# Optimization experiments

Measured on AMD Instinct MI355X. Metric: run time of the kernel, lower is better.

The kernel has to match this reference:

```python
import jax, jax.numpy as jnp
import numpy as np

EMBED_DIM = 1024
NUM_HEADS = 16
HEAD_DIM = EMBED_DIM // NUM_HEADS
WINDOW = 128


def setup_inputs() -> dict:
    key = jax.random.key(0)
    ks = jax.random.split(key, 9)
    B, T, C = 1, 2048, EMBED_DIM
    s = 1.0 / np.sqrt(C)
    inp = {
        "x": jax.random.normal(ks[0], (B, T, C), dtype=jnp.float32),
        "wq": jax.random.normal(ks[1], (C, C), dtype=jnp.float32) * s,
        "bq": jnp.zeros((C,), dtype=jnp.float32),
        "wk": jax.random.normal(ks[2], (C, C), dtype=jnp.float32) * s,
        "bk": jnp.zeros((C,), dtype=jnp.float32),
        "wv": jax.random.normal(ks[3], (C, C), dtype=jnp.float32) * s,
        "bv": jnp.zeros((C,), dtype=jnp.float32),
        "wo": jax.random.normal(ks[4], (C, C), dtype=jnp.float32) * s,
        "bo": jnp.zeros((C,), dtype=jnp.float32),
    }
    return inp


def reference(x, wq, bq, wk, bk, wv, bv, wo, bo):
    B, T, C = x.shape
    H, D, W = NUM_HEADS, HEAD_DIM, WINDOW

    def proj(w, b):
        # torch Linear: y = x @ w.T + b ; -> (B, H, T, D)
        return (x @ w.T + b).reshape(B, T, H, D).transpose(0, 2, 1, 3)

    q = proj(wq, bq)
    k = proj(wk, bk)
    v = proj(wv, bv)

    # window index map: position t attends to keys [t-W+1, t]; zero-padded before 0
    idx = jnp.arange(T)[:, None] + jnp.arange(W)[None, :] - (W - 1)  # (T, W)
    valid = (idx >= 0)
    idxc = jnp.clip(idx, 0, T - 1)

    kw = k[:, :, idxc]                                 # (B, H, T, W, D)
    vw = v[:, :, idxc] * valid[None, None, :, :, None]  # zero padded values

    # zero-key padding gives raw score exactly 0 (inside the softmax)
    scores = jnp.einsum('bhtd,bhtwd->bhtw', q, kw)
    scores = jnp.where(valid[None, None], scores, 0.0) / np.sqrt(D)
    attn = jax.nn.softmax(scores, axis=-1)             # (B, H, T, W)

    ctx = jnp.einsum('bhtw,bhtwd->bhtd', attn, vw)     # (B, H, T, D)
    out = ctx.transpose(0, 2, 1, 3).reshape(B, T, C)
    return out @ wo.T + bo
```

## Files before the change

kernel.cpp:

```cpp
#include <hip/hip_runtime.h>


#define TSEQ 2048
#define CDIM 1024
#define HNUM 16
#define DHEAD 64
#define WWIN 128

typedef __attribute__((ext_vector_type(8))) short bf16x8;
typedef __attribute__((ext_vector_type(4))) float f32x4;

__device__ __forceinline__ unsigned short f2bf(float f) {
  unsigned u = __float_as_uint(f);
  u = (u + 0x7fffu + ((u >> 16) & 1u)) >> 16;
  return (unsigned short)u;
}
__device__ __forceinline__ float bf2f(unsigned short s) {
  return __uint_as_float(((unsigned)s) << 16);
}

__device__ __forceinline__ void gload16(const void* g, void* l) {
  __builtin_amdgcn_global_load_lds(
      (const __attribute__((address_space(1))) unsigned int*)g,
      (__attribute__((address_space(3))) unsigned int*)l, 16, 0, 0);
}

__global__ void split_bf16(const float* s0, const float* s1, const float* s2,
                           const float* s3,
                           unsigned short* h0, unsigned short* h1,
                           unsigned short* h2, unsigned short* h3,
                           unsigned short* l0, unsigned short* l1,
                           unsigned short* l2, unsigned short* l3, int n4) {
  const int z = blockIdx.z;
  const float* __restrict__ src = z == 0 ? s0 : (z == 1 ? s1 : (z == 2 ? s2 : s3));
  unsigned short* __restrict__ h = z == 0 ? h0 : (z == 1 ? h1 : (z == 2 ? h2 : h3));
  unsigned short* __restrict__ l = z == 0 ? l0 : (z == 1 ? l1 : (z == 2 ? l2 : l3));
  const int i = blockIdx.x * 256 + threadIdx.x;
  if (i >= n4) return;
  const float4 v = ((const float4*)src)[i];
  ushort4 hh, ll;
  hh.x = f2bf(v.x); ll.x = f2bf(v.x - bf2f(hh.x));
  hh.y = f2bf(v.y); ll.y = f2bf(v.y - bf2f(hh.y));
  hh.z = f2bf(v.z); ll.z = f2bf(v.z - bf2f(hh.z));
  hh.w = f2bf(v.w); ll.w = f2bf(v.w - bf2f(hh.w));
  ((ushort4*)h)[i] = hh;
  ((ushort4*)l)[i] = ll;
}

__launch_bounds__(256, 2)
__global__ void gemm_mfma_split(const unsigned short* __restrict__ Ah,
                                const unsigned short* __restrict__ Al,
                                const unsigned short* Bh0, const unsigned short* Bh1,
                                const unsigned short* Bh2,
                                const unsigned short* Bl0, const unsigned short* Bl1,
                                const unsigned short* Bl2,
                                const float* bias0, const float* bias1, const float* bias2,
                                float* C0, float* C1, float* C2,
                                int M, int N, int K) {
  const int z = blockIdx.z;
  const unsigned short* __restrict__ Bh = z == 0 ? Bh0 : (z == 1 ? Bh1 : Bh2);
  const unsigned short* __restrict__ Bl = z == 0 ? Bl0 : (z == 1 ? Bl1 : Bl2);
  const float* __restrict__ bias = z == 0 ? bias0 : (z == 1 ? bias1 : bias2);
  float* __restrict__ C = z == 0 ? C0 : (z == 1 ? C1 : C2);

  __shared__ unsigned short lAh[64 * 32], lAl[64 * 32];
  __shared__ unsigned short lBh[128 * 32], lBl[128 * 32];

  const int tid = threadIdx.x;
  const int w = tid >> 6, lane = tid & 63;
  const int wr = w >> 1, wc = w & 1;
  const int bm = blockIdx.y * 64, bn = blockIdx.x * 128;

  const int sA = tid;
  const int rA = sA >> 2;
  const int cA = ((sA & 3) ^ ((rA >> 1) & 3)) * 8;
  const int oA = (w * 64) * 8;
  int srowB[2], scolB[2], soffB[2];
#pragma unroll
  for (int q = 0; q < 2; ++q) {
    const int s = w * 128 + q * 64 + lane;
    const int r = s >> 2;
    srowB[q] = r;
    scolB[q] = ((s & 3) ^ ((r >> 1) & 3)) * 8;
    soffB[q] = (w * 128 + q * 64) * 8;
  }
  int aoff[2], boff[4];
#pragma unroll
  for (int i = 0; i < 2; ++i) {
    const int ra = wr * 32 + i * 16 + (lane & 15);
    aoff[i] = ra * 32 + (((lane >> 4) ^ ((ra >> 1) & 3)) * 8);
  }
#pragma unroll
  for (int j = 0; j < 4; ++j) {
    const int rb = wc * 64 + j * 16 + (lane & 15);
    boff[j] = rb * 32 + (((lane >> 4) ^ ((rb >> 1) & 3)) * 8);
  }

  f32x4 acc[2][4];
#pragma unroll
  for (int i = 0; i < 2; ++i)
#pragma unroll
    for (int j = 0; j < 4; ++j) acc[i][j] = {0.f, 0.f, 0.f, 0.f};

  const unsigned short* gAh = Ah + (size_t)bm * K;
  const unsigned short* gAl = Al + (size_t)bm * K;
  const unsigned short* gBh = Bh + (size_t)bn * K;
  const unsigned short* gBl = Bl + (size_t)bn * K;

  for (int k0 = 0; k0 < K; k0 += 32) {
    {
      const size_t goA = (size_t)rA * K + k0 + cA;
      gload16(gAh + goA, &lAh[oA]);
      gload16(gAl + goA, &lAl[oA]);
    }
#pragma unroll
    for (int q = 0; q < 2; ++q) {
      const size_t go = (size_t)srowB[q] * K + k0 + scolB[q];
      gload16(gBh + go, &lBh[soffB[q]]);
      gload16(gBl + go, &lBl[soffB[q]]);
    }
    __syncthreads();

    bf16x8 fah[2], fal[2], fbh[4], fbl[4];
#pragma unroll
    for (int i = 0; i < 2; ++i) {
      fah[i] = *(const bf16x8*)&lAh[aoff[i]];
      fal[i] = *(const bf16x8*)&lAl[aoff[i]];
    }
#pragma unroll
    for (int j = 0; j < 4; ++j) {
      fbh[j] = *(const bf16x8*)&lBh[boff[j]];
      fbl[j] = *(const bf16x8*)&lBl[boff[j]];
    }
#pragma unroll
    for (int i = 0; i < 2; ++i)
#pragma unroll
      for (int j = 0; j < 4; ++j) {
        acc[i][j] = __builtin_amdgcn_mfma_f32_16x16x32_bf16(fah[i], fbh[j], acc[i][j], 0, 0, 0);
        acc[i][j] = __builtin_amdgcn_mfma_f32_16x16x32_bf16(fah[i], fbl[j], acc[i][j], 0, 0, 0);
        acc[i][j] = __builtin_amdgcn_mfma_f32_16x16x32_bf16(fal[i], fbh[j], acc[i][j], 0, 0, 0);
      }
    __syncthreads();
  }

  const int colb = bn + wc * 64 + (lane & 15);
  const int rowb = bm + wr * 32 + ((lane >> 4) << 2);
#pragma unroll
  for (int j = 0; j < 4; ++j) {
    const int col = colb + j * 16;
    const float bv = bias[col];
#pragma unroll
    for (int i = 0; i < 2; ++i) {
      const int row = rowb + i * 16;
#pragma unroll
      for (int r = 0; r < 4; ++r)
        C[(size_t)(row + r) * N + col] = acc[i][j][r] + bv;
    }
  }
}

__launch_bounds__(256, 2)
__global__ void gemm_bt(const float* __restrict__ A,
                        const float* __restrict__ Bw0, const float* __restrict__ Bw1,
                        const float* __restrict__ Bw2,
                        const float* __restrict__ bias0, const float* __restrict__ bias1,
                        const float* __restrict__ bias2,
                        float* __restrict__ C0, float* __restrict__ C1, float* __restrict__ C2,
                        int M, int N, int K) {
  const int z = blockIdx.z;
  const float* __restrict__ B = (z == 0) ? Bw0 : ((z == 1) ? Bw1 : Bw2);
  const float* __restrict__ bias = (z == 0) ? bias0 : ((z == 1) ? bias1 : bias2);
  float* __restrict__ C = (z == 0) ? C0 : ((z == 1) ? C1 : C2);

  __shared__ float As[16][132];
  __shared__ float Bs[16][132];

  const int tid = threadIdx.x;
  const int tx = tid & 15;
  const int ty = tid >> 4;
  const int bm = blockIdx.y * 128;
  const int bn = blockIdx.x * 128;
  const int lrow = tid >> 2;
  const int lk = (tid & 3) << 2;

  float acc[8][8] = {};

  for (int k0 = 0; k0 < K; k0 += 16) {
#pragma unroll
    for (int r = 0; r < 2; ++r) {
      const int row = (r << 6) + lrow;
      const float4 a4 = *(const float4*)(A + (size_t)(bm + row) * K + k0 + lk);
      As[lk + 0][row] = a4.x; As[lk + 1][row] = a4.y;
      As[lk + 2][row] = a4.z; As[lk + 3][row] = a4.w;
      const float4 b4 = *(const float4*)(B + (size_t)(bn + row) * K + k0 + lk);
      Bs[lk + 0][row] = b4.x; Bs[lk + 1][row] = b4.y;
      Bs[lk + 2][row] = b4.z; Bs[lk + 3][row] = b4.w;
    }
    __syncthreads();
#pragma unroll
    for (int k = 0; k < 16; ++k) {
      float a[8], b[8];
      *(float4*)(a)     = *(const float4*)(&As[k][ty * 8]);
      *(float4*)(a + 4) = *(const float4*)(&As[k][ty * 8 + 4]);
      *(float4*)(b)     = *(const float4*)(&Bs[k][tx * 8]);
      *(float4*)(b + 4) = *(const float4*)(&Bs[k][tx * 8 + 4]);
#pragma unroll
      for (int i = 0; i < 8; ++i)
#pragma unroll
        for (int j = 0; j < 8; ++j)
          acc[i][j] = fmaf(a[i], b[j], acc[i][j]);
    }
    __syncthreads();
  }

#pragma unroll
  for (int i = 0; i < 8; ++i) {
    const int row = bm + ty * 8 + i;
#pragma unroll
    for (int j4 = 0; j4 < 2; ++j4) {
      const int col = bn + tx * 8 + j4 * 4;
      const float4 bb = *(const float4*)(bias + col);
      float4 o;
      o.x = acc[i][j4 * 4 + 0] + bb.x;
      o.y = acc[i][j4 * 4 + 1] + bb.y;
      o.z = acc[i][j4 * 4 + 2] + bb.z;
      o.w = acc[i][j4 * 4 + 3] + bb.w;
      *(float4*)(C + (size_t)row * N + col) = o;
    }
  }
}

__launch_bounds__(512)
__global__ void swa_attn(const float* __restrict__ Q, const float* __restrict__ K,
                         const float* __restrict__ V, float* __restrict__ Of,
                         unsigned short* __restrict__ Oh, unsigned short* __restrict__ Ol,
                         int pack) {
  __shared__ float kb[160 * 64];
  __shared__ float qs[32 * 64];
  __shared__ float ps[8 * 4 * 132];

  const int h = blockIdx.y;
  const int t0 = blockIdx.x * 32;
  const int tid = threadIdx.x;
  const int hoff = h * DHEAD;

  for (int i = tid; i < 160 * 16; i += 512) {
    const int x = i >> 4;
    const int cp = i & 15;
    const int c = cp ^ (x & 15);
    const int key = t0 - (WWIN - 1) + x;
    float4 kv = make_float4(0.f, 0.f, 0.f, 0.f);
    if (key >= 0 && key < TSEQ)
      kv = *(const float4*)(K + (size_t)key * CDIM + hoff + 4 * c);
    *(float4*)&kb[x * 64 + 4 * cp] = kv;
  }
  for (int i = tid; i < 32 * 16; i += 512) {
    const int xq = i >> 4;
    const int c = i & 15;
    *(float4*)&qs[xq * 64 + 4 * c] =
        *(const float4*)(Q + (size_t)(t0 + xq) * CDIM + hoff + 4 * c);
  }
  for (int i = tid; i < 8 * 4 * 132; i += 512) ps[i] = 0.f;
  __syncthreads();

  const int w = tid >> 6;
  const int lane = tid & 63;
  const int q0 = w * 4;

  float inv[4];

#pragma unroll
  for (int q = 0; q < 4; ++q) {
    const int xl = q0 + q + lane;
    const int xm = xl & 15;
    const float* kp0 = kb + xl * 64;
    const float* kp1 = kp0 + 64 * 64;
    const float* qp = qs + (q0 + q) * 64;
    float s0 = 0.f, s1 = 0.f;
#pragma unroll
    for (int dc = 0; dc < 16; ++dc) {
      const float4 qv = *(const float4*)(qp + 4 * dc);
      const int co = 4 * (dc ^ xm);
      const float4 k0 = *(const float4*)(kp0 + co);
      const float4 k1 = *(const float4*)(kp1 + co);
      s0 = fmaf(qv.x, k0.x, fmaf(qv.y, k0.y, fmaf(qv.z, k0.z, fmaf(qv.w, k0.w, s0))));
      s1 = fmaf(qv.x, k1.x, fmaf(qv.y, k1.y, fmaf(qv.z, k1.z, fmaf(qv.w, k1.w, s1))));
    }
    s0 *= 0.125f;
    s1 *= 0.125f;

    float m = fmaxf(s0, s1);
#pragma unroll
    for (int off = 32; off > 0; off >>= 1) m = fmaxf(m, __shfl_xor(m, off));
    const float p0 = __expf(s0 - m);
    const float p1 = __expf(s1 - m);
    float sum = p0 + p1;
#pragma unroll
    for (int off = 32; off > 0; off >>= 1) sum += __shfl_xor(sum, off);
    inv[q] = 1.0f / sum;

    float* psq = ps + (w * 4 + q) * 132;
    psq[q + lane] = p0;
    psq[q + 64 + lane] = p1;
  }

  float accq[4] = {0.f, 0.f, 0.f, 0.f};
  const float* psb = ps + w * 4 * 132;
#pragma unroll 4
  for (int ci = 0; ci < 33; ++ci) {
    const int xr = 4 * ci;
    const float4 pq0 = *(const float4*)(psb + 0 * 132 + xr);
    const float4 pq1 = *(const float4*)(psb + 1 * 132 + xr);
    const float4 pq2 = *(const float4*)(psb + 2 * 132 + xr);
    const float4 pq3 = *(const float4*)(psb + 3 * 132 + xr);
#pragma unroll
    for (int xi = 0; xi < 4; ++xi) {
      const int x = q0 + xr + xi;
      const int key = t0 - (WWIN - 1) + x;
      float vx = 0.f;
      if (key >= 0) {
        const int kc = key < TSEQ ? key : TSEQ - 1;
        vx = V[(size_t)kc * CDIM + hoff + lane];
      }
      const float f0 = (xi == 0) ? pq0.x : (xi == 1) ? pq0.y : (xi == 2) ? pq0.z : pq0.w;
      const float f1 = (xi == 0) ? pq1.x : (xi == 1) ? pq1.y : (xi == 2) ? pq1.z : pq1.w;
      const float f2 = (xi == 0) ? pq2.x : (xi == 1) ? pq2.y : (xi == 2) ? pq2.z : pq2.w;
      const float f3 = (xi == 0) ? pq3.x : (xi == 1) ? pq3.y : (xi == 2) ? pq3.z : pq3.w;
      accq[0] = fmaf(f0, vx, accq[0]);
      accq[1] = fmaf(f1, vx, accq[1]);
      accq[2] = fmaf(f2, vx, accq[2]);
      accq[3] = fmaf(f3, vx, accq[3]);
    }
  }

#pragma unroll
  for (int q = 0; q < 4; ++q) {
    const size_t idx = (size_t)(t0 + q0 + q) * CDIM + hoff + lane;
    const float o = accq[q] * inv[q];
    if (pack) {
      const unsigned short hv = f2bf(o);
      Oh[idx] = hv;
      Ol[idx] = f2bf(o - bf2f(hv));
    } else {
      Of[idx] = o;
    }
  }
}

extern "C" void kernel_launch(void* const* d_in, const int* in_sizes, int n_in,
                              void* d_out, int out_size, void* d_ws, size_t ws_size,
                              hipStream_t stream) {
  const float* x  = (const float*)d_in[0];
  const float* wq = (const float*)d_in[1];
  const float* bq = (const float*)d_in[2];
  const float* wk = (const float*)d_in[3];
  const float* bk = (const float*)d_in[4];
  const float* wv = (const float*)d_in[5];
  const float* bv = (const float*)d_in[6];
  const float* wo = (const float*)d_in[7];
  const float* bo = (const float*)d_in[8];
  float* out = (float*)d_out;

  const size_t MB = 1024 * 1024;
  const size_t NTOK = (size_t)TSEQ * CDIM;

  if (ws_size >= 48 * MB) {
    char* wsb = (char*)d_ws;
    unsigned short* Whq = (unsigned short*)(wsb + 0 * MB);
    unsigned short* Wlq = (unsigned short*)(wsb + 2 * MB);
    unsigned short* Whk = (unsigned short*)(wsb + 4 * MB);
    unsigned short* Wlk = (unsigned short*)(wsb + 6 * MB);
    unsigned short* Whv = (unsigned short*)(wsb + 8 * MB);
    unsigned short* Wlv = (unsigned short*)(wsb + 10 * MB);
    unsigned short* Who = (unsigned short*)(wsb + 12 * MB);
    unsigned short* Wlo = (unsigned short*)(wsb + 14 * MB);
    float* Qw = (float*)(wsb + 16 * MB);
    float* Kw = (float*)(wsb + 24 * MB);
    float* Vw = (float*)(wsb + 32 * MB);
    unsigned short* Ch = (unsigned short*)(wsb + 40 * MB);
    unsigned short* Cl = (unsigned short*)(wsb + 44 * MB);
    unsigned short* Xh = (unsigned short*)d_out;
    unsigned short* Xl = Xh + NTOK;

    {
      dim3 gx((int)(NTOK / 4 / 256), 1, 1);
      split_bf16<<<gx, 256, 0, stream>>>(x, x, x, x, Xh, Xh, Xh, Xh,
                                         Xl, Xl, Xl, Xl, (int)(NTOK / 4));
      const int wn4 = CDIM * CDIM / 4;
      dim3 gw(wn4 / 256, 1, 4);
      split_bf16<<<gw, 256, 0, stream>>>(wq, wk, wv, wo, Whq, Whk, Whv, Who,
                                         Wlq, Wlk, Wlv, Wlo, wn4);
    }

    dim3 gqkv(CDIM / 128, TSEQ / 64, 3);
    gemm_mfma_split<<<gqkv, 256, 0, stream>>>(Xh, Xl, Whq, Whk, Whv, Wlq, Wlk, Wlv,
                                              bq, bk, bv, Qw, Kw, Vw,
                                              TSEQ, CDIM, CDIM);

    dim3 gattn(TSEQ / 32, HNUM);
    swa_attn<<<gattn, 512, 0, stream>>>(Qw, Kw, Vw, (float*)0, Ch, Cl, 1);

    dim3 gout(CDIM / 128, TSEQ / 64, 1);
    gemm_mfma_split<<<gout, 256, 0, stream>>>(Ch, Cl, Who, Who, Who, Wlo, Wlo, Wlo,
                                              bo, bo, bo, out, out, out,
                                              TSEQ, CDIM, CDIM);
  } else {
    float* Qw = (float*)d_ws;
    float* Kw = Qw + NTOK;
    float* Vw = Kw + NTOK;
    float* Cw = Vw + NTOK;

    dim3 gqkv(CDIM / 128, TSEQ / 128, 3);
    gemm_bt<<<gqkv, 256, 0, stream>>>(x, wq, wk, wv, bq, bk, bv, Qw, Kw, Vw,
                                      TSEQ, CDIM, CDIM);

    dim3 gattn(TSEQ / 32, HNUM);
    swa_attn<<<gattn, 512, 0, stream>>>(Qw, Kw, Vw, Cw, (unsigned short*)0,
                                        (unsigned short*)0, 0);

    dim3 gout(CDIM / 128, TSEQ / 128, 1);
    gemm_bt<<<gout, 256, 0, stream>>>(Cw, wo, wo, wo, bo, bo, bo, out, out, out,
                                      TSEQ, CDIM, CDIM);
  }
}
```

Before: 217.2 us.

## Reuse K loads across four queries in attention; narrow output GEMM tile

The attention score loop now has each lane load its K rows once and reuse them across all four queries a wave handles, instead of reloading Q and K per query. A third K row covers the window shift, and a per-lane select picks which score applies. Separately, the GEMM is templated on its N tile width, and the output projection uses 64-wide tiles so its grid has more blocks to fill the GPU. The costs are higher register pressure in attention and less operand reuse per block in the output GEMM.

```diff
diff --git a/kernel.cpp b/kernel.cpp
--- a/kernel.cpp
+++ b/kernel.cpp
@@ -47,6 +47,7 @@
   ((ushort4*)l)[i] = ll;
 }
 
+template <int BN>
 __launch_bounds__(256, 2)
 __global__ void gemm_mfma_split(const unsigned short* __restrict__ Ah,
                                 const unsigned short* __restrict__ Al,
@@ -57,6 +58,8 @@
                                 const float* bias0, const float* bias1, const float* bias2,
                                 float* C0, float* C1, float* C2,
                                 int M, int N, int K) {
+  constexpr int NJ = BN / 32;
+  constexpr int QB = BN / 64;
   const int z = blockIdx.z;
   const unsigned short* __restrict__ Bh = z == 0 ? Bh0 : (z == 1 ? Bh1 : Bh2);
   const unsigned short* __restrict__ Bl = z == 0 ? Bl0 : (z == 1 ? Bl1 : Bl2);
@@ -64,43 +67,43 @@
   float* __restrict__ C = z == 0 ? C0 : (z == 1 ? C1 : C2);
 
   __shared__ unsigned short lAh[64 * 32], lAl[64 * 32];
-  __shared__ unsigned short lBh[128 * 32], lBl[128 * 32];
+  __shared__ unsigned short lBh[BN * 32], lBl[BN * 32];
 
   const int tid = threadIdx.x;
   const int w = tid >> 6, lane = tid & 63;
   const int wr = w >> 1, wc = w & 1;
-  const int bm = blockIdx.y * 64, bn = blockIdx.x * 128;
+  const int bm = blockIdx.y * 64, bn = blockIdx.x * BN;
 
   const int sA = tid;
   const int rA = sA >> 2;
   const int cA = ((sA & 3) ^ ((rA >> 1) & 3)) * 8;
   const int oA = (w * 64) * 8;
-  int srowB[2], scolB[2], soffB[2];
-#pragma unroll
-  for (int q = 0; q < 2; ++q) {
-    const int s = w * 128 + q * 64 + lane;
+  int srowB[QB], scolB[QB], soffB[QB];
+#pragma unroll
+  for (int q = 0; q < QB; ++q) {
+    const int s = w * 64 * QB + q * 64 + lane;
     const int r = s >> 2;
     srowB[q] = r;
     scolB[q] = ((s & 3) ^ ((r >> 1) & 3)) * 8;
-    soffB[q] = (w * 128 + q * 64) * 8;
-  }
-  int aoff[2], boff[4];
+    soffB[q] = (w * 64 * QB + q * 64) * 8;
+  }
+  int aoff[2], boff[NJ];
 #pragma unroll
   for (int i = 0; i < 2; ++i) {
     const int ra = wr * 32 + i * 16 + (lane & 15);
     aoff[i] = ra * 32 + (((lane >> 4) ^ ((ra >> 1) & 3)) * 8);
   }
 #pragma unroll
-  for (int j = 0; j < 4; ++j) {
-    const int rb = wc * 64 + j * 16 + (lane & 15);
+  for (int j = 0; j < NJ; ++j) {
+    const int rb = wc * (BN / 2) + j * 16 + (lane & 15);
     boff[j] = rb * 32 + (((lane >> 4) ^ ((rb >> 1) & 3)) * 8);
   }
 
-  f32x4 acc[2][4];
+  f32x4 acc[2][NJ];
 #pragma unroll
   for (int i = 0; i < 2; ++i)
 #pragma unroll
-    for (int j = 0; j < 4; ++j) acc[i][j] = {0.f, 0.f, 0.f, 0.f};
+    for (int j = 0; j < NJ; ++j) acc[i][j] = {0.f, 0.f, 0.f, 0.f};
 
   const unsigned short* gAh = Ah + (size_t)bm * K;
   const unsigned short* gAl = Al + (size_t)bm * K;
@@ -114,28 +117,28 @@
       gload16(gAl + goA, &lAl[oA]);
     }
 #pragma unroll
-    for (int q = 0; q < 2; ++q) {
+    for (int q = 0; q < QB; ++q) {
       const size_t go = (size_t)srowB[q] * K + k0 + scolB[q];
       gload16(gBh + go, &lBh[soffB[q]]);
       gload16(gBl + go, &lBl[soffB[q]]);
     }
     __syncthreads();
 
-    bf16x8 fah[2], fal[2], fbh[4], fbl[4];
+    bf16x8 fah[2], fal[2], fbh[NJ], fbl[NJ];
 #pragma unroll
     for (int i = 0; i < 2; ++i) {
       fah[i] = *(const bf16x8*)&lAh[aoff[i]];
       fal[i] = *(const bf16x8*)&lAl[aoff[i]];
     }
 #pragma unroll
-    for (int j = 0; j < 4; ++j) {
+    for (int j = 0; j < NJ; ++j) {
       fbh[j] = *(const bf16x8*)&lBh[boff[j]];
       fbl[j] = *(const bf16x8*)&lBl[boff[j]];
     }
 #pragma unroll
     for (int i = 0; i < 2; ++i)
 #pragma unroll
-      for (int j = 0; j < 4; ++j) {
+      for (int j = 0; j < NJ; ++j) {
         acc[i][j] = __builtin_amdgcn_mfma_f32_16x16x32_bf16(fah[i], fbh[j], acc[i][j], 0, 0, 0);
         acc[i][j] = __builtin_amdgcn_mfma_f32_16x16x32_bf16(fah[i], fbl[j], acc[i][j], 0, 0, 0);
         acc[i][j] = __builtin_amdgcn_mfma_f32_16x16x32_bf16(fal[i], fbh[j], acc[i][j], 0, 0, 0);
@@ -143,10 +146,10 @@
     __syncthreads();
   }
 
-  const int colb = bn + wc * 64 + (lane & 15);
+  const int colb = bn + wc * (BN / 2) + (lane & 15);
   const int rowb = bm + wr * 32 + ((lane >> 4) << 2);
 #pragma unroll
-  for (int j = 0; j < 4; ++j) {
+  for (int j = 0; j < NJ; ++j) {
     const int col = colb + j * 16;
     const float bv = bias[col];
 #pragma unroll
@@ -264,44 +267,56 @@
   __syncthreads();
 
   const int w = tid >> 6;
-  const int lane = tid & 63;
+  const int L = tid & 63;
   const int q0 = w * 4;
 
+  const int x0 = q0 + L;
+  const int xm = x0 & 15;
+  const float* kp0 = kb + x0 * 64;
+  const float* kp1 = kp0 + 64 * 64;
+  const int x2 = (x0 + 128 < 160) ? (x0 + 128) : 159;
+  const float* kp2 = kb + x2 * 64;
+  const float* qp = qs + q0 * 64;
+
+  float s0[4] = {0.f, 0.f, 0.f, 0.f};
+  float s1[4] = {0.f, 0.f, 0.f, 0.f};
+  float s2[4] = {0.f, 0.f, 0.f, 0.f};
+#pragma unroll
+  for (int dc = 0; dc < 16; ++dc) {
+    const int co = 4 * (dc ^ xm);
+    const float4 k0 = *(const float4*)(kp0 + co);
+    const float4 k1 = *(const float4*)(kp1 + co);
+    const float4 k2 = *(const float4*)(kp2 + co);
+#pragma unroll
+    for (int q = 0; q < 4; ++q) {
+      const float4 qv = *(const float4*)(qp + q * 64 + 4 * dc);
+      s0[q] = fmaf(qv.x, k0.x, fmaf(qv.y, k0.y, fmaf(qv.z, k0.z, fmaf(qv.w, k0.w, s0[q]))));
+      s1[q] = fmaf(qv.x, k1.x, fmaf(qv.y, k1.y, fmaf(qv.z, k1.z, fmaf(qv.w, k1.w, s1[q]))));
+      if (q > 0)
+        s2[q] = fmaf(qv.x, k2.x, fmaf(qv.y, k2.y, fmaf(qv.z, k2.z, fmaf(qv.w, k2.w, s2[q]))));
+    }
+  }
+
   float inv[4];
-
 #pragma unroll
   for (int q = 0; q < 4; ++q) {
-    const int xl = q0 + q + lane;
-    const int xm = xl & 15;
-    const float* kp0 = kb + xl * 64;
-    const float* kp1 = kp0 + 64 * 64;
-    const float* qp = qs + (q0 + q) * 64;
-    float s0 = 0.f, s1 = 0.f;
-#pragma unroll
-    for (int dc = 0; dc < 16; ++dc) {
-      const float4 qv = *(const float4*)(qp + 4 * dc);
-      const int co = 4 * (dc ^ xm);
-      const float4 k0 = *(const float4*)(kp0 + co);
-      const float4 k1 = *(const float4*)(kp1 + co);
-      s0 = fmaf(qv.x, k0.x, fmaf(qv.y, k0.y, fmaf(qv.z, k0.z, fmaf(qv.w, k0.w, s0))));
-      s1 = fmaf(qv.x, k1.x, fmaf(qv.y, k1.y, fmaf(qv.z, k1.z, fmaf(qv.w, k1.w, s1))));
-    }
-    s0 *= 0.125f;
-    s1 *= 0.125f;
-
-    float m = fmaxf(s0, s1);
+    const bool lo = (L >= q);
+    const float sa = (lo ? s0[q] : s2[q]) * 0.125f;
+    const float sb = s1[q] * 0.125f;
+
+    float m = fmaxf(sa, sb);
 #pragma unroll
     for (int off = 32; off > 0; off >>= 1) m = fmaxf(m, __shfl_xor(m, off));
-    const float p0 = __expf(s0 - m);
-    const float p1 = __expf(s1 - m);
-    float sum = p0 + p1;
+    const float pa = __expf(sa - m);
+    const float pb = __expf(sb - m);
+    float sum = pa + pb;
 #pragma unroll
     for (int off = 32; off > 0; off >>= 1) sum += __shfl_xor(sum, off);
     inv[q] = 1.0f / sum;
 
     float* psq = ps + (w * 4 + q) * 132;
-    psq[q + lane] = p0;
-    psq[q + 64 + lane] = p1;
+    psq[lo ? L : (128 + L)] = pa;
+    psq[64 + L] = pb;
   }
 
   float accq[4] = {0.f, 0.f, 0.f, 0.f};
@@ -320,7 +335,7 @@
       float vx = 0.f;
       if (key >= 0) {
         const int kc = key < TSEQ ? key : TSEQ - 1;
-        vx = V[(size_t)kc * CDIM + hoff + lane];
+        vx = V[(size_t)kc * CDIM + hoff + L];
       }
       const float f0 = (xi == 0) ? pq0.x : (xi == 1) ? pq0.y : (xi == 2) ? pq0.z : pq0.w;
       const float f1 = (xi == 0) ? pq1.x : (xi == 1) ? pq1.y : (xi == 2) ? pq1.z : pq1.w;
@@ -335,7 +350,7 @@
 
 #pragma unroll
   for (int q = 0; q < 4; ++q) {
-    const size_t idx = (size_t)(t0 + q0 + q) * CDIM + hoff + lane;
+    const size_t idx = (size_t)(t0 + q0 + q) * CDIM + hoff + L;
     const float o = accq[q] * inv[q];
     if (pack) {
       const unsigned short hv = f2bf(o);
@@ -393,17 +408,19 @@
     }
 
     dim3 gqkv(CDIM / 128, TSEQ / 64, 3);
-    gemm_mfma_split<<<gqkv, 256, 0, stream>>>(Xh, Xl, Whq, Whk, Whv, Wlq, Wlk, Wlv,
-                                              bq, bk, bv, Qw, Kw, Vw,
-                                              TSEQ, CDIM, CDIM);
+    gemm_mfma_split<128><<<gqkv, 256, 0, stream>>>(Xh, Xl, Whq, Whk, Whv,
+                                                   Wlq, Wlk, Wlv,
+                                                   bq, bk, bv, Qw, Kw, Vw,
+                                                   TSEQ, CDIM, CDIM);
 
     dim3 gattn(TSEQ / 32, HNUM);
     swa_attn<<<gattn, 512, 0, stream>>>(Qw, Kw, Vw, (float*)0, Ch, Cl, 1);
 
-    dim3 gout(CDIM / 128, TSEQ / 64, 1);
-    gemm_mfma_split<<<gout, 256, 0, stream>>>(Ch, Cl, Who, Who, Who, Wlo, Wlo, Wlo,
-                                              bo, bo, bo, out, out, out,
-                                              TSEQ, CDIM, CDIM);
+    dim3 gout(CDIM / 64, TSEQ / 64, 1);
+    gemm_mfma_split<64><<<gout, 256, 0, stream>>>(Ch, Cl, Who, Who, Who,
+                                                  Wlo, Wlo, Wlo,
+                                                  bo, bo, bo, out, out, out,
+                                                  TSEQ, CDIM, CDIM);
   } else {
     float* Qw = (float*)d_ws;
     float* Kw = Qw + NTOK;
```

New measurement: 202.2 us. 1.07x faster.
